# Performance work log

Measured on AMD Instinct MI355X. Metric: run time of the kernel, lower is better.

Reference implementation:

```python
import jax, jax.numpy as jnp
import numpy as np

GRID_H = 128
GRID_W = 128
D = 64
K = 16
HID = 4 * D
EPS = 1e-5


def _hankel_filters(L, k):
    # Hankel matrix Z[i,j] = 2 / ((i+j)^3 - (i+j)), 1-indexed; top-k eigvecs scaled by eigval^0.25
    idx = np.arange(1, L + 1)
    s = (idx[:, None] + idx[None, :]).astype(np.float64)
    Z = 2.0 / (s ** 3 - s)
    vals, vecs = np.linalg.eigh(Z)
    phi = vecs[:, -k:] * (vals[-k:] ** 0.25)
    return jnp.asarray(phi, dtype=jnp.float32)  # (L, k)


def setup_inputs() -> dict:
    key = jax.random.key(0)
    ks = jax.random.split(key, 9)
    def n(k, shape, scale=0.02):
        return jax.random.normal(k, shape, dtype=jnp.float32) * scale
    return {
        'v': jax.random.normal(ks[0], (4, GRID_H * GRID_W, D), dtype=jnp.float32),
        'gamma_row': jnp.ones((D,), jnp.float32), 'beta_row': jnp.zeros((D,), jnp.float32),
        'gamma_col': jnp.ones((D,), jnp.float32), 'beta_col': jnp.zeros((D,), jnp.float32),
        'm_plus_row': n(ks[1], (K, D, D)), 'm_minus_row': n(ks[2], (K, D, D)),
        'm_plus_col': n(ks[3], (K, D, D)), 'm_minus_col': n(ks[4], (K, D, D)),
        'w1_row': n(ks[5], (D, HID)), 'b1_row': jnp.zeros((HID,), jnp.float32),
        'w2_row': n(ks[6], (HID, D)), 'b2_row': jnp.zeros((D,), jnp.float32),
        'w1_col': n(ks[7], (D, HID)), 'b1_col': jnp.zeros((HID,), jnp.float32),
        'w2_col': n(ks[8], (HID, D)), 'b2_col': jnp.zeros((D,), jnp.float32),
        'phi_row': _hankel_filters(GRID_W, K),
        'phi_col': _hankel_filters(GRID_H, K),
    }


def _layernorm(x, g, b):
    mu = jnp.mean(x, -1, keepdims=True)
    var = jnp.mean((x - mu) ** 2, -1, keepdims=True)
    return (x - mu) * jax.lax.rsqrt(var + EPS) * g + b


def _ministu(x, phi, mp, mm, w1, b1, w2, b2):
    # x: (B, L, d); phi: (L, K). Causal FFT conv with pos/neg featurization, then per-filter projection + MLP.
    B, L, d = x.shape
    nfft = 2 * L
    sgn = jnp.where(jnp.arange(L) % 2 == 0, 1.0, -1.0).astype(x.dtype)  # (-1)^t
    pf = jnp.fft.rfft(phi, n=nfft, axis=0)                         # (F, K)
    xf = jnp.fft.rfft(x, n=nfft, axis=1)                           # (B, F, d)
    xmf = jnp.fft.rfft(x * sgn[None, :, None], n=nfft, axis=1)     # (B, F, d)
    up = jnp.fft.irfft(pf[None, :, :, None] * xf[:, :, None, :], n=nfft, axis=1)[:, :L]   # (B, L, K, d)
    um = jnp.fft.irfft(pf[None, :, :, None] * xmf[:, :, None, :], n=nfft, axis=1)[:, :L]
    um = um * sgn[None, :, None, None]
    spec = jnp.einsum('blkd,kde->ble', up, mp) + jnp.einsum('blkd,kde->ble', um, mm)
    h = jax.nn.gelu(spec @ w1 + b1)
    return h @ w2 + b2


def reference(v, gamma_row, beta_row, gamma_col, beta_col,
              m_plus_row, m_minus_row, m_plus_col, m_minus_col,
              w1_row, b1_row, w2_row, b2_row,
              w1_col, b1_col, w2_col, b2_col,
              phi_row, phi_col):
    B, N, d = v.shape
    x = v.reshape(B, GRID_H, GRID_W, d)
    # row pass: (B*H, W, d)
    xr = x.reshape(B * GRID_H, GRID_W, d)
    xr = xr + _ministu(_layernorm(xr, gamma_row, beta_row), phi_row,
                       m_plus_row, m_minus_row, w1_row, b1_row, w2_row, b2_row)
    x = xr.reshape(B, GRID_H, GRID_W, d).transpose(0, 2, 1, 3)
    # col pass: (B*W, H, d)
    xc = x.reshape(B * GRID_W, GRID_H, d)
    xc = xc + _ministu(_layernorm(xc, gamma_col, beta_col), phi_col,
                       m_plus_col, m_minus_col, w1_col, b1_col, w2_col, b2_col)
    x = xc.reshape(B, GRID_W, GRID_H, d).transpose(0, 2, 1, 3)
    return x.reshape(B, N, d)
```

## Files before the change

### kernel.cpp

```cpp
#include <hip/hip_runtime.h>
#include <hip/hip_fp8.h>

typedef __attribute__((ext_vector_type(8))) short bf16x8;
typedef __attribute__((ext_vector_type(4))) float f32x4;

__device__ __forceinline__ float gelu_fast(float x) {
    const float u = 0.7978845608028654f * x * (1.0f + 0.044715f * x * x);
    return x * __builtin_amdgcn_rcpf(1.0f + __expf(-2.0f * u));
}

__device__ __forceinline__ unsigned short f2bf(float x) {
    union { float f; unsigned int u; } v; v.f = x;
    unsigned int r = v.u + 0x7FFF + ((v.u >> 16) & 1);
    return (unsigned short)(r >> 16);
}

__device__ __forceinline__ unsigned char f2fp8(float x) {
    __hip_fp8_e4m3 h(x);
    return *(unsigned char*)&h;
}

__global__ __launch_bounds__(256) void init_kernel(const float* __restrict__ phi_r, const float* __restrict__ mp_r,
                                                   const float* __restrict__ mm_r, unsigned char* __restrict__ GfR,
                                                   const float* __restrict__ phi_c, const float* __restrict__ mp_c,
                                                   const float* __restrict__ mm_c, unsigned char* __restrict__ GfC,
                                                   const float* __restrict__ w1r, const float* __restrict__ w1c,
                                                   const float* __restrict__ w2r, const float* __restrict__ w2c,
                                                   unsigned short* __restrict__ w1tr, unsigned short* __restrict__ w1tc,
                                                   unsigned short* __restrict__ w2tr, unsigned short* __restrict__ w2tc) {
    const int bid = blockIdx.x, tid = threadIdx.x;
    __shared__ float phis[256];
    __shared__ unsigned char tile8[4096];
    if (bid < 256) {
        const int side = bid >> 7, rem = bid & 127;
        const int chunk = rem >> 3, s0 = (rem & 7) * 16;
        const float* phi = side ? phi_c : phi_r;
        const float* mp  = side ? mp_c  : mp_r;
        const float* mm  = side ? mm_c  : mm_r;
        unsigned char* Gf8 = side ? GfC : GfR;
        const int i = chunk * 256 + tid;
        float pe[16], po[16];
#pragma unroll
        for (int k = 0; k < 16; ++k) {
            const float a = mp[k * 4096 + i];
            const float b = mm[k * 4096 + i];
            pe[k] = a + b; po[k] = a - b;
        }
        phis[tid] = phi[s0 * 16 + tid];
        __syncthreads();
        const int e = tid & 63, dl = tid >> 6;
        const int d0 = chunk * 4;
        const int kk = d0 >> 5, g3 = (d0 >> 3) & 3, jl0 = d0 & 7;
#pragma unroll
        for (int sb = 0; sb < 16; ++sb) {
            const int s = s0 + sb;
            const float* pk = &phis[sb * 16];
            float acc = 0.0f;
            if (s & 1) {
#pragma unroll
                for (int k = 0; k < 16; ++k) acc += pk[k] * po[k];
            } else {
#pragma unroll
                for (int k = 0; k < 16; ++k) acc += pk[k] * pe[k];
            }
            tile8[sb * 256 + e * 4 + dl] = f2fp8(acc * 32.0f);
        }
        __syncthreads();
#pragma unroll
        for (int it = 0; it < 4; ++it) {
            const int p = it * 256 + tid;
            const int sb = p >> 6, ee = p & 63;
            unsigned int v = *(const unsigned int*)&tile8[sb * 256 + ee * 4];
            *(unsigned int*)&Gf8[(size_t)(s0 + sb) * 4096 + (((ee >> 4) << 1) + kk) * 512 +
                                 (g3 * 16 + (ee & 15)) * 8 + jl0] = v;
        }
    } else {
        const int b = bid - 256;
        if (b < 2) {
            const float* w1 = b ? w1c : w1r;
            unsigned short* dst = b ? w1tc : w1tr;
            const int n = tid;
            for (int k = 0; k < 64; ++k) dst[n * 64 + k] = f2bf(w1[k * 256 + n]);
        } else {
            const float* w2 = (b == 3) ? w2c : w2r;
            unsigned short* dst = (b == 3) ? w2tc : w2tr;
            const int n = tid & 63, kq = tid >> 6;
            for (int kk2 = 0; kk2 < 64; ++kk2) {
                const int k = kq * 64 + kk2;
                dst[n * 256 + k] = f2bf(w2[k * 64 + n]);
            }
        }
    }
}

#define SPEC_BODY(RR, BC, BN)                                                        \
    {                                                                                \
        const int s_ = 4 * (RR) + w;                                                 \
        if ((RR) < 31) {                                                             \
            const unsigned char* gq = Gf8 + (size_t)(s_ + 4) * 4096 + lane * 8;      \
            _Pragma("unroll")                                                        \
            for (int f = 0; f < 8; ++f) BN[f] = *(const long*)(gq + f * 512);        \
        }                                                                            \
        const int jmin_ = __builtin_amdgcn_readfirstlane(s_ >> 4);                   \
        __builtin_amdgcn_s_setprio(1);                                               \
        _Pragma("unroll")                                                            \
        for (int j = 0; j < 8; ++j) {                                                \
            if (j >= jmin_) {                                                        \
                const int row_ = 16 + 16 * j - s_ + m;                               \
                const int c0_ = (g ^ (row_ & 7)) << 3;                               \
                const int ab_ = row_ * 64;                                           \
                long a0_ = *(const long*)&lds8[ab_ + c0_];                           \
                long a1_ = *(const long*)&lds8[ab_ + (c0_ ^ 32)];                    \
                _Pragma("unroll")                                                    \
                for (int nt = 0; nt < 4; ++nt) {                                     \
                    acc[j][nt] = __builtin_amdgcn_mfma_f32_16x16x32_fp8_fp8(a0_, BC[2 * nt], acc[j][nt], 0, 0, 0);     \
                    acc[j][nt] = __builtin_amdgcn_mfma_f32_16x16x32_fp8_fp8(a1_, BC[2 * nt + 1], acc[j][nt], 0, 0, 0); \
                }                                                                    \
            }                                                                        \
        }                                                                            \
        __builtin_amdgcn_s_setprio(0);                                               \
    }

__global__ __launch_bounds__(256, 2) void fused_kernel(const float* __restrict__ xin,
                                                       float* __restrict__ xout,
                                                       const unsigned char* __restrict__ Gf8,
                                                       const unsigned short* __restrict__ w1t,
                                                       const unsigned short* __restrict__ w2t,
                                                       const float* __restrict__ b1,
                                                       const float* __restrict__ b2,
                                                       const float* __restrict__ gamma,
                                                       const float* __restrict__ beta,
                                                       int rmul, int tmul) {
    __shared__ unsigned char lds8[51200];
    unsigned short* const ldsu = (unsigned short*)lds8;
    const int tid = threadIdx.x;
    const int w = tid >> 6, lane = tid & 63;
    const int seq = blockIdx.x;
    const int m = lane & 15, g = lane >> 4;
    const int bb = seq >> 7, rr = seq & 127;
    const size_t base = (size_t)bb * 1048576 + (size_t)rr * (size_t)rmul;

    *(unsigned int*)&lds8[tid * 4] = 0u;

    long Ba[8], Bb[8];
    {
        const unsigned char* gq = Gf8 + (size_t)w * 4096 + lane * 8;
#pragma unroll
        for (int f = 0; f < 8; ++f) Ba[f] = *(const long*)(gq + f * 512);
    }

    {
        const float gl = gamma[lane], bl = beta[lane];
        float xv[32];
#pragma unroll
        for (int ti = 0; ti < 32; ++ti)
            xv[ti] = xin[base + (size_t)(w * 32 + ti) * tmul + lane];
#pragma unroll
        for (int ti = 0; ti < 32; ++ti) {
            const int t = w * 32 + ti;
            float s1 = xv[ti];
#pragma unroll
            for (int mm2 = 32; mm2 >= 1; mm2 >>= 1) s1 += __shfl_xor(s1, mm2);
            const float mu = s1 * (1.0f / 64.0f);
            const float dv = xv[ti] - mu;
            float s2 = dv * dv;
#pragma unroll
            for (int mm2 = 32; mm2 >= 1; mm2 >>= 1) s2 += __shfl_xor(s2, mm2);
            const float rstd = rsqrtf(s2 * (1.0f / 64.0f) + 1e-5f);
            const float nv = dv * rstd * gl + bl;
            lds8[(t + 16) * 64 + (((lane >> 3) ^ (t & 7)) << 3) + (lane & 7)] = f2fp8(nv);
        }
    }
    __syncthreads();

    f32x4 acc[8][4];
#pragma unroll
    for (int j = 0; j < 8; ++j)
#pragma unroll
        for (int nt = 0; nt < 4; ++nt) {
            f32x4 z = {0.0f, 0.0f, 0.0f, 0.0f};
            acc[j][nt] = z;
        }
    for (int rp = 0; rp < 16; ++rp) {
        SPEC_BODY(2 * rp,     Ba, Bb);
        SPEC_BODY(2 * rp + 1, Bb, Ba);
    }

    char* const scrA = (char*)lds8 + 18432;
    char* const scrB = (char*)lds8 + 34816;
    if (w == 1 || w == 3) {
        char* pb = (w == 1 ? scrA : scrB) + lane * 16;
#pragma unroll
        for (int j = 0; j < 4; ++j)
#pragma unroll
            for (int nt = 0; nt < 4; ++nt)
                *(f32x4*)(pb + (j * 4 + nt) * 1024) = acc[j][nt];
    }
    bf16x8 bw1a[2][2], bw1b[2][2];
    float b1va[2], b1vb[2];
#pragma unroll
    for (int nt = 0; nt < 2; ++nt) {
        const int col0 = w * 32 + nt * 16 + m;
#pragma unroll
        for (int j = 0; j < 2; ++j) {
            bw1a[nt][j] = *(const bf16x8*)&w1t[col0 * 64 + (4 * j + g) * 8];
            bw1b[nt][j] = *(const bf16x8*)&w1t[(128 + col0) * 64 + (4 * j + g) * 8];
        }
        b1va[nt] = b1[col0];
        b1vb[nt] = b1[128 + col0];
    }
    __syncthreads();
    if (w == 0 || w == 2) {
        const char* pb = (w == 0 ? scrA : scrB) + lane * 16;
#pragma unroll
        for (int j = 0; j < 4; ++j)
#pragma unroll
            for (int nt = 0; nt < 4; ++nt)
                acc[j][nt] += *(const f32x4*)(pb + (j * 4 + nt) * 1024);
    }
    __syncthreads();
    if (w == 1 || w == 3) {
        char* pb = (w == 1 ? scrA : scrB) + lane * 16;
#pragma unroll
        for (int j = 4; j < 8; ++j)
#pragma unroll
            for (int nt = 0; nt < 4; ++nt)
                *(f32x4*)(pb + ((j - 4) * 4 + nt) * 1024) = acc[j][nt];
    }
    __syncthreads();
    if (w == 0 || w == 2) {
        const char* pb = (w == 0 ? scrA : scrB) + lane * 16;
#pragma unroll
        for (int j = 4; j < 8; ++j)
#pragma unroll
            for (int nt = 0; nt < 4; ++nt)
                acc[j][nt] += *(const f32x4*)(pb + ((j - 4) * 4 + nt) * 1024);
        if (w == 0) {
#pragma unroll
            for (int j = 4; j < 8; ++j)
#pragma unroll
                for (int nt = 0; nt < 4; ++nt)
                    *(f32x4*)(scrA + ((j - 4) * 4 + nt) * 1024 + lane * 16) = acc[j][nt];
        } else {
#pragma unroll
            for (int j = 0; j < 4; ++j)
#pragma unroll
                for (int nt = 0; nt < 4; ++nt)
                    *(f32x4*)(scrB + (j * 4 + nt) * 1024 + lane * 16) = acc[j][nt];
        }
    }
    __syncthreads();
    if (w == 0) {
#pragma unroll
        for (int j = 0; j < 4; ++j)
#pragma unroll
            for (int nt = 0; nt < 4; ++nt) {
                acc[j][nt] += *(const f32x4*)(scrB + (j * 4 + nt) * 1024 + lane * 16);
#pragma unroll
                for (int rv = 0; rv < 4; ++rv) {
                    const int row = j * 16 + 4 * g + rv;
                    const int col = nt * 16 + m;
                    ldsu[row * 64 + (((col >> 3) ^ (row & 7)) << 3) + (col & 7)] = f2bf(acc[j][nt][rv] * 0.03125f);
                }
            }
    } else if (w == 2) {
#pragma unroll
        for (int j = 4; j < 8; ++j)
#pragma unroll
            for (int nt = 0; nt < 4; ++nt) {
                acc[j][nt] += *(const f32x4*)(scrA + ((j - 4) * 4 + nt) * 1024 + lane * 16);
#pragma unroll
                for (int rv = 0; rv < 4; ++rv) {
                    const int row = j * 16 + 4 * g + rv;
                    const int col = nt * 16 + m;
                    ldsu[row * 64 + (((col >> 3) ^ (row & 7)) << 3) + (col & 7)] = f2bf(acc[j][nt][rv] * 0.03125f);
                }
            }
    }
    __syncthreads();

    float xr[2][4][4];
#pragma unroll
    for (int mt = 0; mt < 2; ++mt)
#pragma unroll
        for (int nt = 0; nt < 4; ++nt)
#pragma unroll
            for (int rv = 0; rv < 4; ++rv)
                xr[mt][nt][rv] = xin[base + (size_t)((w + 4 * mt) * 16 + 4 * g + rv) * tmul + nt * 16 + m];

    float b2v[4];
#pragma unroll
    for (int nt = 0; nt < 4; ++nt) b2v[nt] = b2[nt * 16 + m];
    f32x4 acc2[2][4];
#pragma unroll
    for (int mt = 0; mt < 2; ++mt)
#pragma unroll
        for (int nt = 0; nt < 4; ++nt) {
            f32x4 z = {b2v[nt], b2v[nt], b2v[nt], b2v[nt]};
            acc2[mt][nt] = z;
        }

#pragma unroll
    for (int half = 0; half < 2; ++half) {
        f32x4 acc1[8][2];
#pragma unroll
        for (int mt = 0; mt < 8; ++mt)
#pragma unroll
            for (int nt = 0; nt < 2; ++nt) {
                const float bv = half ? b1vb[nt] : b1va[nt];
                f32x4 z = {bv, bv, bv, bv};
                acc1[mt][nt] = z;
            }
        __builtin_amdgcn_s_setprio(1);
#pragma unroll
        for (int mt = 0; mt < 8; ++mt) {
            const int row = mt * 16 + m;
            const int c0 = (g ^ (row & 7)) << 3;
            bf16x8 a0 = *(const bf16x8*)&ldsu[row * 64 + c0];
            bf16x8 a1 = *(const bf16x8*)&ldsu[row * 64 + (c0 ^ 32)];
#pragma unroll
            for (int nt = 0; nt < 2; ++nt) {
                const bf16x8 w0f = half ? bw1b[nt][0] : bw1a[nt][0];
                const bf16x8 w1f = half ? bw1b[nt][1] : bw1a[nt][1];
                acc1[mt][nt] = __builtin_amdgcn_mfma_f32_16x16x32_bf16(a0, w0f, acc1[mt][nt], 0, 0, 0);
                acc1[mt][nt] = __builtin_amdgcn_mfma_f32_16x16x32_bf16(a1, w1f, acc1[mt][nt], 0, 0, 0);
            }
        }
        __builtin_amdgcn_s_setprio(0);
#pragma unroll
        for (int mt = 0; mt < 8; ++mt)
#pragma unroll
            for (int nt = 0; nt < 2; ++nt) {
                const int col = w * 32 + nt * 16 + m;
                const int c = col >> 3, jj = col & 7;
#pragma unroll
                for (int rv = 0; rv < 4; ++rv) {
                    const int row = mt * 16 + 4 * g + rv;
                    ldsu[8192 + row * 128 + ((c ^ (row & 7)) << 3) + jj] = f2bf(gelu_fast(acc1[mt][nt][rv]));
                }
            }
        __syncthreads();

        __builtin_amdgcn_s_setprio(1);
#pragma unroll
        for (int j = 0; j < 4; ++j) {
            bf16x8 aa[2];
#pragma unroll
            for (int mt = 0; mt < 2; ++mt) {
                const int row = (w + 4 * mt) * 16 + m;
                aa[mt] = *(const bf16x8*)&ldsu[8192 + row * 128 + (((4 * j + g) ^ (row & 7)) << 3)];
            }
#pragma unroll
            for (int nt = 0; nt < 4; ++nt) {
                const int row = nt * 16 + m;
                bf16x8 bfr = *(const bf16x8*)&w2t[row * 256 + half * 128 + (4 * j + g) * 8];
                acc2[0][nt] = __builtin_amdgcn_mfma_f32_16x16x32_bf16(aa[0], bfr, acc2[0][nt], 0, 0, 0);
                acc2[1][nt] = __builtin_amdgcn_mfma_f32_16x16x32_bf16(aa[1], bfr, acc2[1][nt], 0, 0, 0);
            }
        }
        __builtin_amdgcn_s_setprio(0);
        if (half == 0) __syncthreads();
    }

#pragma unroll
    for (int mt = 0; mt < 2; ++mt)
#pragma unroll
        for (int nt = 0; nt < 4; ++nt)
#pragma unroll
            for (int rv = 0; rv < 4; ++rv) {
                const int row = (w + 4 * mt) * 16 + 4 * g + rv;
                const int col = nt * 16 + m;
                const size_t xi = base + (size_t)row * tmul + col;
                xout[xi] = xr[mt][nt][rv] + acc2[mt][nt][rv];
            }
}

extern "C" void kernel_launch(void* const* d_in, const int* in_sizes, int n_in,
                              void* d_out, int out_size, void* d_ws, size_t ws_size,
                              hipStream_t stream) {
    const float* v         = (const float*)d_in[0];
    const float* gamma_row = (const float*)d_in[1];
    const float* beta_row  = (const float*)d_in[2];
    const float* gamma_col = (const float*)d_in[3];
    const float* beta_col  = (const float*)d_in[4];
    const float* mp_row    = (const float*)d_in[5];
    const float* mm_row    = (const float*)d_in[6];
    const float* mp_col    = (const float*)d_in[7];
    const float* mm_col    = (const float*)d_in[8];
    const float* w1_row    = (const float*)d_in[9];
    const float* b1_row    = (const float*)d_in[10];
    const float* w2_row    = (const float*)d_in[11];
    const float* b2_row    = (const float*)d_in[12];
    const float* w1_col    = (const float*)d_in[13];
    const float* b1_col    = (const float*)d_in[14];
    const float* w2_col    = (const float*)d_in[15];
    const float* b2_col    = (const float*)d_in[16];
    const float* phi_row   = (const float*)d_in[17];
    const float* phi_col   = (const float*)d_in[18];
    float* out = (float*)d_out;
    char* ws   = (char*)d_ws;

    unsigned char* GfR   = (unsigned char*)ws;
    unsigned char* GfC   = (unsigned char*)(ws + (1u << 20));
    unsigned short* w1tR = (unsigned short*)(ws + (2u << 20));
    unsigned short* w2tR = (unsigned short*)(ws + (2u << 20) + 32768);
    unsigned short* w1tC = (unsigned short*)(ws + (2u << 20) + 65536);
    unsigned short* w2tC = (unsigned short*)(ws + (2u << 20) + 98304);

    init_kernel<<<260, 256, 0, stream>>>(phi_row, mp_row, mm_row, GfR,
                                         phi_col, mp_col, mm_col, GfC,
                                         w1_row, w1_col, w2_row, w2_col,
                                         w1tR, w1tC, w2tR, w2tC);

    fused_kernel<<<512, 256, 0, stream>>>(v, out, GfR, w1tR, w2tR, b1_row, b2_row,
                                          gamma_row, beta_row, 8192, 64);
    fused_kernel<<<512, 256, 0, stream>>>(out, out, GfC, w1tC, w2tC, b1_col, b2_col,
                                          gamma_col, beta_col, 64, 8192);
}
```

Before: 116.0 us.

## Switch spectral conv MFMA to 16x16x128 scaled fp8 instruction with pairwise shifts

New measurement: 100.1 us (median of 2 runs). 13.7% less time.

```diff
diff --git a/kernel.cpp b/kernel.cpp
--- a/kernel.cpp
+++ b/kernel.cpp
@@ -3,6 +3,8 @@
 
 typedef __attribute__((ext_vector_type(8))) short bf16x8;
 typedef __attribute__((ext_vector_type(4))) float f32x4;
+typedef __attribute__((ext_vector_type(8))) int i32x8;
+typedef __attribute__((ext_vector_type(4))) unsigned int u32x4;
 
 __device__ __forceinline__ float gelu_fast(float x) {
     const float u = 0.7978845608028654f * x * (1.0f + 0.044715f * x * x);
@@ -50,7 +52,6 @@
         __syncthreads();
         const int e = tid & 63, dl = tid >> 6;
         const int d0 = chunk * 4;
-        const int kk = d0 >> 5, g3 = (d0 >> 3) & 3, jl0 = d0 & 7;
 #pragma unroll
         for (int sb = 0; sb < 16; ++sb) {
             const int s = s0 + sb;
@@ -71,8 +72,12 @@
             const int p = it * 256 + tid;
             const int sb = p >> 6, ee = p & 63;
             unsigned int v = *(const unsigned int*)&tile8[sb * 256 + ee * 4];
-            *(unsigned int*)&Gf8[(size_t)(s0 + sb) * 4096 + (((ee >> 4) << 1) + kk) * 512 +
-                                 (g3 * 16 + (ee & 15)) * 8 + jl0] = v;
+            const int s = s0 + sb;
+            const int sp = s >> 1, hi = s & 1;
+            const int k0 = 64 * hi + d0;
+            const int gg = k0 >> 5, kk0 = k0 & 31;
+            *(unsigned int*)&Gf8[(size_t)sp * 8192 + (ee >> 4) * 2048 +
+                                 ((ee & 15) + 16 * gg) * 32 + kk0] = v;
         }
     } else {
         const int b = bid - 256;
@@ -95,27 +100,28 @@
 
 #define SPEC_BODY(RR, BC, BN)                                                        \
     {                                                                                \
-        const int s_ = 4 * (RR) + w;                                                 \
-        if ((RR) < 31) {                                                             \
-            const unsigned char* gq = Gf8 + (size_t)(s_ + 4) * 4096 + lane * 8;      \
+        const int sp_ = 4 * (RR) + w;                                                \
+        if ((RR) < 15) {                                                             \
+            const unsigned char* gq = Gf8 + (size_t)(sp_ + 4) * 8192 + lane * 32;    \
             _Pragma("unroll")                                                        \
-            for (int f = 0; f < 8; ++f) BN[f] = *(const long*)(gq + f * 512);        \
+            for (int f = 0; f < 4; ++f) BN[f] = *(const i32x8*)(gq + f * 2048);      \
         }                                                                            \
-        const int jmin_ = __builtin_amdgcn_readfirstlane(s_ >> 4);                   \
+        const int jmin_ = __builtin_amdgcn_readfirstlane((2 * sp_ + 1) >> 4);        \
         __builtin_amdgcn_s_setprio(1);                                               \
         _Pragma("unroll")                                                            \
         for (int j = 0; j < 8; ++j) {                                                \
             if (j >= jmin_) {                                                        \
-                const int row_ = 16 + 16 * j - s_ + m;                               \
-                const int c0_ = (g ^ (row_ & 7)) << 3;                               \
-                const int ab_ = row_ * 64;                                           \
-                long a0_ = *(const long*)&lds8[ab_ + c0_];                           \
-                long a1_ = *(const long*)&lds8[ab_ + (c0_ ^ 32)];                    \
+                const int srow = 16 + 16 * j - 2 * sp_ - (g >> 1) + m;               \
+                const int cb_ = 2 * (g & 1);                                         \
+                u32x4 lo_ = *(const u32x4*)&lds8[srow * 64 + ((cb_ ^ (srow & 3)) << 4)];       \
+                u32x4 hi_ = *(const u32x4*)&lds8[srow * 64 + (((cb_ + 1) ^ (srow & 3)) << 4)]; \
+                i32x8 av;                                                            \
+                av[0] = lo_[0]; av[1] = lo_[1]; av[2] = lo_[2]; av[3] = lo_[3];      \
+                av[4] = hi_[0]; av[5] = hi_[1]; av[6] = hi_[2]; av[7] = hi_[3];      \
                 _Pragma("unroll")                                                    \
-                for (int nt = 0; nt < 4; ++nt) {                                     \
-                    acc[j][nt] = __builtin_amdgcn_mfma_f32_16x16x32_fp8_fp8(a0_, BC[2 * nt], acc[j][nt], 0, 0, 0);     \
-                    acc[j][nt] = __builtin_amdgcn_mfma_f32_16x16x32_fp8_fp8(a1_, BC[2 * nt + 1], acc[j][nt], 0, 0, 0); \
-                }                                                                    \
+                for (int nt = 0; nt < 4; ++nt)                                       \
+                    acc[j][nt] = __builtin_amdgcn_mfma_scale_f32_16x16x128_f8f6f4(   \
+                        av, BC[nt], acc[j][nt], 0, 0, 0, 0x7F7F7F7F, 0, 0x7F7F7F7F); \
             }                                                                        \
         }                                                                            \
         __builtin_amdgcn_s_setprio(0);                                               \
@@ -142,11 +148,11 @@
 
     *(unsigned int*)&lds8[tid * 4] = 0u;
 
-    long Ba[8], Bb[8];
+    i32x8 Ba[4], Bb[4];
     {
-        const unsigned char* gq = Gf8 + (size_t)w * 4096 + lane * 8;
-#pragma unroll
-        for (int f = 0; f < 8; ++f) Ba[f] = *(const long*)(gq + f * 512);
+        const unsigned char* gq = Gf8 + (size_t)w * 8192 + lane * 32;
+#pragma unroll
+        for (int f = 0; f < 4; ++f) Ba[f] = *(const i32x8*)(gq + f * 2048);
     }
 
     {
@@ -168,7 +174,7 @@
             for (int mm2 = 32; mm2 >= 1; mm2 >>= 1) s2 += __shfl_xor(s2, mm2);
             const float rstd = rsqrtf(s2 * (1.0f / 64.0f) + 1e-5f);
             const float nv = dv * rstd * gl + bl;
-            lds8[(t + 16) * 64 + (((lane >> 3) ^ (t & 7)) << 3) + (lane & 7)] = f2fp8(nv);
+            lds8[(t + 16) * 64 + (((lane >> 4) ^ (t & 3)) << 4) + (lane & 15)] = f2fp8(nv);
         }
     }
     __syncthreads();
@@ -181,7 +187,7 @@
             f32x4 z = {0.0f, 0.0f, 0.0f, 0.0f};
             acc[j][nt] = z;
         }
-    for (int rp = 0; rp < 16; ++rp) {
+    for (int rp = 0; rp < 8; ++rp) {
         SPEC_BODY(2 * rp,     Ba, Bb);
         SPEC_BODY(2 * rp + 1, Bb, Ba);
     }
```
